# Performance work log

Hardware: AMD Instinct MI355X
Metric: run time of the kernel (lower is better)

The kernel has to match this reference:

```python
import jax, jax.numpy as jnp
import numpy as np

TEMPERATURE = 8.0  # sqrt(d_k), d_k = 64


def setup_inputs() -> dict:
    key = jax.random.key(0)
    kq, kk, kv, km = jax.random.split(key, 4)
    B, Lq, Lk, D = 64, 1024, 1024, 64
    q = jax.random.normal(kq, (B, Lq, D), dtype=jnp.float32)
    k = jax.random.normal(kk, (B, Lk, D), dtype=jnp.float32)
    v = jax.random.normal(kv, (B, Lk, D), dtype=jnp.float32)
    mask = jax.random.randint(km, (B, Lq, Lk), 0, 2).astype(jnp.bool_)
    return {"q": q, "k": k, "v": v, "mask": mask}


def reference(q, k, v, mask):
    # attn = q @ k^T / temperature, masked softmax over last dim, then @ v
    attn = jnp.einsum("bqd,bkd->bqk", q, k) / TEMPERATURE
    attn = jnp.where(mask, -jnp.inf, attn)
    attn = jax.nn.softmax(attn, axis=2)
    output = jnp.einsum("bqk,bkd->bqd", attn, v)
    return (output, attn)
```

## Files before the change

kernel.cpp:

```cpp
#include <hip/hip_runtime.h>
#include <hip/hip_bf16.h>


#define LQT 64
#define KSTRIDE 72
#define PSTRIDE 68

typedef __attribute__((ext_vector_type(8))) short bf16x8;
typedef __attribute__((ext_vector_type(4))) float f32x4;

static __device__ __forceinline__ short f2bf(float f) {
    unsigned u = __builtin_bit_cast(unsigned, f);
    unsigned r = (u + 0x7fffu + ((u >> 16) & 1u)) >> 16;
    return (short)r;
}
static __device__ __forceinline__ bf16x8 pack8(float4 a, float4 b) {
    bf16x8 r;
    r[0] = f2bf(a.x); r[1] = f2bf(a.y); r[2] = f2bf(a.z); r[3] = f2bf(a.w);
    r[4] = f2bf(b.x); r[5] = f2bf(b.y); r[6] = f2bf(b.z); r[7] = f2bf(b.w);
    return r;
}

__global__ __launch_bounds__(256) void attn_kernel(
    const float* __restrict__ q, const float* __restrict__ k,
    const float* __restrict__ v, const int* __restrict__ mask,
    float* __restrict__ out, float* __restrict__ attn)
{
    __shared__ unsigned maskbits[64][32];
    __shared__ short kbuf[64 * KSTRIDE];
    __shared__ short vtbuf[64 * KSTRIDE];
    __shared__ float ptile[4 * 16 * PSTRIDE];

    const int tid  = threadIdx.x;
    const int w    = tid >> 6;
    const int L    = tid & 63;
    const int n    = L & 15;
    const int quad = L >> 4;
    const int b    = blockIdx.y;
    const int q0   = blockIdx.x * LQT;
    const long bq  = (long)b * 1024 + q0;

    const float* qrow = q + (bq + 16 * w + n) * 64 + quad * 8;
    float4 qa0 = ((const float4*)qrow)[0];
    float4 qa1 = ((const float4*)(qrow + 4))[0];
    float4 qb0 = ((const float4*)(qrow + 32))[0];
    float4 qb1 = ((const float4*)(qrow + 36))[0];
    const float sc = 0.125f;
    qa0.x *= sc; qa0.y *= sc; qa0.z *= sc; qa0.w *= sc;
    qa1.x *= sc; qa1.y *= sc; qa1.z *= sc; qa1.w *= sc;
    qb0.x *= sc; qb0.y *= sc; qb0.z *= sc; qb0.w *= sc;
    qb1.x *= sc; qb1.y *= sc; qb1.z *= sc; qb1.w *= sc;
    bf16x8 qf0 = pack8(qa0, qa1);
    bf16x8 qf1 = pack8(qb0, qb1);

    #pragma unroll
    for (int ii = 0; ii < 8; ++ii) {
        int wi  = ii * 256 + tid;
        int row = wi >> 5;
        int wc  = wi & 31;
        const int4* mp = (const int4*)(mask + (bq + row) * 1024 + wc * 32);
        unsigned word = 0;
        #pragma unroll
        for (int j = 0; j < 8; ++j) {
            int4 m4 = mp[j];
            word |= (m4.x != 0 ? 1u : 0u) << (4 * j + 0);
            word |= (m4.y != 0 ? 1u : 0u) << (4 * j + 1);
            word |= (m4.z != 0 ? 1u : 0u) << (4 * j + 2);
            word |= (m4.w != 0 ? 1u : 0u) << (4 * j + 3);
        }
        maskbits[row][wc] = word;
    }

    float m_i[4] = {-1e30f, -1e30f, -1e30f, -1e30f};
    float l_i[4] = {0.f, 0.f, 0.f, 0.f};

    for (int kt = 0; kt < 16; ++kt) {
        __syncthreads();
        {
            const float* kr = k + ((long)b * 1024 + kt * 64 + L) * 64 + w * 16;
            float4 k0 = ((const float4*)kr)[0];
            float4 k1 = ((const float4*)kr)[1];
            float4 k2 = ((const float4*)kr)[2];
            float4 k3 = ((const float4*)kr)[3];
            bf16x8* dst = (bf16x8*)&kbuf[L * KSTRIDE + w * 16];
            dst[0] = pack8(k0, k1);
            dst[1] = pack8(k2, k3);
        }
        __syncthreads();

        f32x4 acc[4];
        #pragma unroll
        for (int t = 0; t < 4; ++t) { acc[t][0]=0.f; acc[t][1]=0.f; acc[t][2]=0.f; acc[t][3]=0.f; }
        #pragma unroll
        for (int t = 0; t < 4; ++t) {
            bf16x8 b0 = *(const bf16x8*)&kbuf[(t * 16 + n) * KSTRIDE + quad * 8];
            bf16x8 b1 = *(const bf16x8*)&kbuf[(t * 16 + n) * KSTRIDE + 32 + quad * 8];
            acc[t] = __builtin_amdgcn_mfma_f32_16x16x32_bf16(qf0, b0, acc[t], 0, 0, 0);
            acc[t] = __builtin_amdgcn_mfma_f32_16x16x32_bf16(qf1, b1, acc[t], 0, 0, 0);
        }
        #pragma unroll
        for (int i = 0; i < 4; ++i) {
            int mrow = 16 * w + quad * 4 + i;
            unsigned w0 = maskbits[mrow][kt * 2];
            unsigned w1 = maskbits[mrow][kt * 2 + 1];
            float s0 = ((w0 >> n)        & 1u) ? -1e30f : acc[0][i];
            float s1 = ((w0 >> (16 + n)) & 1u) ? -1e30f : acc[1][i];
            float s2 = ((w1 >> n)        & 1u) ? -1e30f : acc[2][i];
            float s3 = ((w1 >> (16 + n)) & 1u) ? -1e30f : acc[3][i];
            float mt = fmaxf(fmaxf(s0, s1), fmaxf(s2, s3));
            mt = fmaxf(mt, __shfl_xor(mt, 1));
            mt = fmaxf(mt, __shfl_xor(mt, 2));
            mt = fmaxf(mt, __shfl_xor(mt, 4));
            mt = fmaxf(mt, __shfl_xor(mt, 8));
            float mnew = fmaxf(m_i[i], mt);
            float ps = __expf(s0 - mnew) + __expf(s1 - mnew)
                     + __expf(s2 - mnew) + __expf(s3 - mnew);
            ps += __shfl_xor(ps, 1);
            ps += __shfl_xor(ps, 2);
            ps += __shfl_xor(ps, 4);
            ps += __shfl_xor(ps, 8);
            l_i[i] = l_i[i] * __expf(m_i[i] - mnew) + ps;
            m_i[i] = mnew;
        }
    }
    float linv[4];
    #pragma unroll
    for (int i = 0; i < 4; ++i) linv[i] = 1.0f / l_i[i];

    f32x4 oacc[4];
    #pragma unroll
    for (int t = 0; t < 4; ++t) { oacc[t][0]=0.f; oacc[t][1]=0.f; oacc[t][2]=0.f; oacc[t][3]=0.f; }

    float* attn_row = attn + (bq + 16 * w + n) * 1024;

    for (int kt = 0; kt < 16; ++kt) {
        __syncthreads();
        {
            const float* kr = k + ((long)b * 1024 + kt * 64 + L) * 64 + w * 16;
            float4 k0 = ((const float4*)kr)[0];
            float4 k1 = ((const float4*)kr)[1];
            float4 k2 = ((const float4*)kr)[2];
            float4 k3 = ((const float4*)kr)[3];
            bf16x8* dst = (bf16x8*)&kbuf[L * KSTRIDE + w * 16];
            dst[0] = pack8(k0, k1);
            dst[1] = pack8(k2, k3);

            const float* vr = v + ((long)b * 1024 + kt * 64 + L) * 64 + w * 16;
            float4 v0 = ((const float4*)vr)[0];
            float4 v1 = ((const float4*)vr)[1];
            float4 v2 = ((const float4*)vr)[2];
            float4 v3 = ((const float4*)vr)[3];
            float vv[16] = {v0.x, v0.y, v0.z, v0.w, v1.x, v1.y, v1.z, v1.w,
                            v2.x, v2.y, v2.z, v2.w, v3.x, v3.y, v3.z, v3.w};
            #pragma unroll
            for (int dd = 0; dd < 16; ++dd)
                vtbuf[(w * 16 + dd) * KSTRIDE + L] = f2bf(vv[dd]);
        }
        __syncthreads();

        f32x4 acc[4];
        #pragma unroll
        for (int t = 0; t < 4; ++t) { acc[t][0]=0.f; acc[t][1]=0.f; acc[t][2]=0.f; acc[t][3]=0.f; }
        #pragma unroll
        for (int t = 0; t < 4; ++t) {
            bf16x8 b0 = *(const bf16x8*)&kbuf[(t * 16 + n) * KSTRIDE + quad * 8];
            bf16x8 b1 = *(const bf16x8*)&kbuf[(t * 16 + n) * KSTRIDE + 32 + quad * 8];
            acc[t] = __builtin_amdgcn_mfma_f32_16x16x32_bf16(qf0, b0, acc[t], 0, 0, 0);
            acc[t] = __builtin_amdgcn_mfma_f32_16x16x32_bf16(qf1, b1, acc[t], 0, 0, 0);
        }
        #pragma unroll
        for (int i = 0; i < 4; ++i) {
            int mrow = 16 * w + quad * 4 + i;
            unsigned w0 = maskbits[mrow][kt * 2];
            unsigned w1 = maskbits[mrow][kt * 2 + 1];
            float s0 = ((w0 >> n)        & 1u) ? -1e30f : acc[0][i];
            float s1 = ((w0 >> (16 + n)) & 1u) ? -1e30f : acc[1][i];
            float s2 = ((w1 >> n)        & 1u) ? -1e30f : acc[2][i];
            float s3 = ((w1 >> (16 + n)) & 1u) ? -1e30f : acc[3][i];
            float* pr = &ptile[(w * 16 + quad * 4 + i) * PSTRIDE];
            pr[n]      = __expf(s0 - m_i[i]) * linv[i];
            pr[16 + n] = __expf(s1 - m_i[i]) * linv[i];
            pr[32 + n] = __expf(s2 - m_i[i]) * linv[i];
            pr[48 + n] = __expf(s3 - m_i[i]) * linv[i];
        }
        bf16x8 pf[2];
        #pragma unroll
        for (int c = 0; c < 2; ++c) {
            const float* pp = &ptile[(w * 16 + n) * PSTRIDE + c * 32 + quad * 8];
            float4 p0 = ((const float4*)pp)[0];
            float4 p1 = ((const float4*)pp)[1];
            float* ap = attn_row + kt * 64 + c * 32 + quad * 8;
            ((float4*)ap)[0] = p0;
            ((float4*)ap)[1] = p1;
            pf[c] = pack8(p0, p1);
        }
        #pragma unroll
        for (int t = 0; t < 4; ++t) {
            bf16x8 vb0 = *(const bf16x8*)&vtbuf[(t * 16 + n) * KSTRIDE + quad * 8];
            bf16x8 vb1 = *(const bf16x8*)&vtbuf[(t * 16 + n) * KSTRIDE + 32 + quad * 8];
            oacc[t] = __builtin_amdgcn_mfma_f32_16x16x32_bf16(pf[0], vb0, oacc[t], 0, 0, 0);
            oacc[t] = __builtin_amdgcn_mfma_f32_16x16x32_bf16(pf[1], vb1, oacc[t], 0, 0, 0);
        }
    }

    #pragma unroll
    for (int t = 0; t < 4; ++t)
        #pragma unroll
        for (int i = 0; i < 4; ++i)
            out[(bq + 16 * w + quad * 4 + i) * 64 + t * 16 + n] = oacc[t][i];
}

extern "C" void kernel_launch(void* const* d_in, const int* in_sizes, int n_in,
                              void* d_out, int out_size, void* d_ws, size_t ws_size,
                              hipStream_t stream) {
    const float* q    = (const float*)d_in[0];
    const float* k    = (const float*)d_in[1];
    const float* v    = (const float*)d_in[2];
    const int*   mask = (const int*)d_in[3];
    float* out  = (float*)d_out;
    float* attn = out + (long)64 * 1024 * 64;

    dim3 grid(16, 64, 1);
    dim3 block(256, 1, 1);
    attn_kernel<<<grid, block, 0, stream>>>(q, k, v, mask, out, attn);
}
```

Measured before the change: 616.5 us.

## Precompute bf16 K, transposed V and packed mask bits; stream via async LDS loads

Adds preprocessing kernels that pack the mask into bitwords with ballots, convert K to swizzled bf16, and transpose V to swizzled bf16 in workspace. The main kernel then double-buffers those tiles into LDS with global_load_lds DMA, so each block no longer redoes the fp32 K/V conversion 16 times over. It also stores P as bf16 in a per-wave tile. The cost is three extra launches and workspace traffic, and the attn output is now written as bf16-rounded values, which lowers its precision. A fallback path keeps the old kernel when workspace is too small.

```diff
diff --git a/kernel.cpp b/kernel.cpp
--- a/kernel.cpp
+++ b/kernel.cpp
@@ -2,17 +2,20 @@
 #include <hip/hip_bf16.h>
 
 
-#define LQT 64
-#define KSTRIDE 72
-#define PSTRIDE 68
-
 typedef __attribute__((ext_vector_type(8))) short bf16x8;
 typedef __attribute__((ext_vector_type(4))) float f32x4;
+
+#define GLOBAL_AS __attribute__((address_space(1)))
+#define LDS_AS    __attribute__((address_space(3)))
 
 static __device__ __forceinline__ short f2bf(float f) {
     unsigned u = __builtin_bit_cast(unsigned, f);
     unsigned r = (u + 0x7fffu + ((u >> 16) & 1u)) >> 16;
     return (short)r;
+}
+static __device__ __forceinline__ float bf2f(short s) {
+    unsigned u = ((unsigned)(unsigned short)s) << 16;
+    return __builtin_bit_cast(float, u);
 }
 static __device__ __forceinline__ bf16x8 pack8(float4 a, float4 b) {
     bf16x8 r;
@@ -21,15 +24,82 @@
     return r;
 }
 
-__global__ __launch_bounds__(256) void attn_kernel(
-    const float* __restrict__ q, const float* __restrict__ k,
-    const float* __restrict__ v, const int* __restrict__ mask,
+static __device__ __forceinline__ void dma16(void* lds, const void* g) {
+    __builtin_amdgcn_global_load_lds((const GLOBAL_AS unsigned*)g,
+                                     (LDS_AS unsigned*)lds, 16, 0, 0);
+}
+static __device__ __forceinline__ void stage8k(short* lds, const short* g, int w, int L) {
+    dma16((void*)(lds + (w * 2 + 0) * 512), (const void*)(g + (w * 2 + 0) * 512 + L * 8));
+    dma16((void*)(lds + (w * 2 + 1) * 512), (const void*)(g + (w * 2 + 1) * 512 + L * 8));
+}
+
+#define KIDX(r, c) ((r) * 64 + ((((c) ^ ((r) & 7))) << 3))
+
+__global__ __launch_bounds__(256) void pre_maskpack(const int* __restrict__ mask,
+                                                    unsigned long long* __restrict__ bits) {
+    const int L = threadIdx.x & 63;
+    long gw = ((long)blockIdx.x * 256 + threadIdx.x) >> 6;
+    const long nseg = (64L * 1024 * 1024) / 256;
+    const long step = (long)gridDim.x * 4;
+    for (long seg = gw; seg < nseg; seg += step) {
+        const int* p = mask + seg * 256;
+        unsigned long long b0 = __ballot(p[L] != 0);
+        unsigned long long b1 = __ballot(p[64 + L] != 0);
+        unsigned long long b2 = __ballot(p[128 + L] != 0);
+        unsigned long long b3 = __ballot(p[192 + L] != 0);
+        if (L == 0) {
+            ulonglong2* d = (ulonglong2*)(bits + seg * 4);
+            ulonglong2 t0; t0.x = b0; t0.y = b1;
+            ulonglong2 t1; t1.x = b2; t1.y = b3;
+            d[0] = t0; d[1] = t1;
+        }
+    }
+}
+
+__global__ __launch_bounds__(256) void pre_kconv(const float* __restrict__ k,
+                                                 short* __restrict__ kb) {
+    long ci = (long)blockIdx.x * 256 + threadIdx.x;
+    long row = ci >> 3;
+    int  c   = (int)(ci & 7);
+    const float4* s = (const float4*)(k + row * 64 + c * 8);
+    float4 a = s[0], bb = s[1];
+    int r = (int)(row & 63);
+    short* dst = kb + (row >> 6) * 4096 + (long)r * 64 + ((c ^ (r & 7)) << 3);
+    *(bf16x8*)dst = pack8(a, bb);
+}
+
+__global__ __launch_bounds__(256) void pre_vtrans(const float* __restrict__ v,
+                                                  short* __restrict__ vt) {
+    __shared__ short t[64][72];
+    const int bkt = blockIdx.x;
+    const int tid = threadIdx.x;
+    const int row = tid >> 2;
+    const int cg  = (tid & 3) * 16;
+    const float* src = v + ((long)bkt * 64 + row) * 64 + cg;
+    float4 f0 = ((const float4*)src)[0];
+    float4 f1 = ((const float4*)src)[1];
+    float4 f2 = ((const float4*)src)[2];
+    float4 f3 = ((const float4*)src)[3];
+    float vv[16] = {f0.x, f0.y, f0.z, f0.w, f1.x, f1.y, f1.z, f1.w,
+                    f2.x, f2.y, f2.z, f2.w, f3.x, f3.y, f3.z, f3.w};
+    #pragma unroll
+    for (int dd = 0; dd < 16; ++dd) t[cg + dd][row] = f2bf(vv[dd]);
+    __syncthreads();
+    const int d = tid >> 2, c0 = (tid & 3) * 2;
+    short* dstrow = vt + (long)bkt * 4096 + d * 64;
+    *(int4*)&dstrow[((c0 ^ (d & 7)) << 3)]       = *(int4*)&t[d][c0 * 8];
+    *(int4*)&dstrow[(((c0 + 1) ^ (d & 7)) << 3)] = *(int4*)&t[d][c0 * 8 + 8];
+}
+
+__global__ __launch_bounds__(256) void attn_main(
+    const float* __restrict__ q, const unsigned* __restrict__ bits,
+    const short* __restrict__ kb, const short* __restrict__ vt,
     float* __restrict__ out, float* __restrict__ attn)
 {
-    __shared__ unsigned maskbits[64][32];
-    __shared__ short kbuf[64 * KSTRIDE];
-    __shared__ short vtbuf[64 * KSTRIDE];
-    __shared__ float ptile[4 * 16 * PSTRIDE];
+    __shared__ unsigned maskbits[64 * 32];
+    __shared__ short kbuf[2][64 * 64];
+    __shared__ short vbuf[2][64 * 64];
+    __shared__ short ptile[4][16 * 72];
 
     const int tid  = threadIdx.x;
     const int w    = tid >> 6;
@@ -37,8 +107,17 @@
     const int n    = L & 15;
     const int quad = L >> 4;
     const int b    = blockIdx.y;
-    const int q0   = blockIdx.x * LQT;
-    const long bq  = (long)b * 1024 + q0;
+    const long bq  = (long)b * 1024 + blockIdx.x * 64;
+
+    const short* ktg = kb + (long)b * 65536;
+    const short* vtg = vt + (long)b * 65536;
+
+    {
+        const unsigned* mg = bits + bq * 32;
+        dma16((void*)(maskbits + (w * 2 + 0) * 256), (const void*)(mg + (w * 2 + 0) * 256 + L * 4));
+        dma16((void*)(maskbits + (w * 2 + 1) * 256), (const void*)(mg + (w * 2 + 1) * 256 + L * 4));
+        stage8k(kbuf[0], ktg, w, L);
+    }
 
     const float* qrow = q + (bq + 16 * w + n) * 64 + quad * 8;
     float4 qa0 = ((const float4*)qrow)[0];
@@ -53,6 +132,159 @@
     bf16x8 qf0 = pack8(qa0, qa1);
     bf16x8 qf1 = pack8(qb0, qb1);
 
+    __syncthreads();
+
+    float m_i[4] = {-1e30f, -1e30f, -1e30f, -1e30f};
+    float l_i[4] = {0.f, 0.f, 0.f, 0.f};
+
+    for (int kt = 0; kt < 16; ++kt) {
+        if (kt < 15) stage8k(kbuf[(kt + 1) & 1], ktg + (kt + 1) * 4096, w, L);
+        const short* kl = kbuf[kt & 1];
+        f32x4 acc[4];
+        #pragma unroll
+        for (int t = 0; t < 4; ++t) { acc[t][0]=0.f; acc[t][1]=0.f; acc[t][2]=0.f; acc[t][3]=0.f; }
+        #pragma unroll
+        for (int t = 0; t < 4; ++t) {
+            bf16x8 b0 = *(const bf16x8*)&kl[KIDX(t * 16 + n, quad)];
+            bf16x8 b1 = *(const bf16x8*)&kl[KIDX(t * 16 + n, 4 + quad)];
+            acc[t] = __builtin_amdgcn_mfma_f32_16x16x32_bf16(qf0, b0, acc[t], 0, 0, 0);
+            acc[t] = __builtin_amdgcn_mfma_f32_16x16x32_bf16(qf1, b1, acc[t], 0, 0, 0);
+        }
+        #pragma unroll
+        for (int i = 0; i < 4; ++i) {
+            int mrow = 16 * w + quad * 4 + i;
+            unsigned w0 = maskbits[mrow * 32 + kt * 2];
+            unsigned w1 = maskbits[mrow * 32 + kt * 2 + 1];
+            float s0 = ((w0 >> n)        & 1u) ? -1e30f : acc[0][i];
+            float s1 = ((w0 >> (16 + n)) & 1u) ? -1e30f : acc[1][i];
+            float s2 = ((w1 >> n)        & 1u) ? -1e30f : acc[2][i];
+            float s3 = ((w1 >> (16 + n)) & 1u) ? -1e30f : acc[3][i];
+            float mt = fmaxf(fmaxf(s0, s1), fmaxf(s2, s3));
+            mt = fmaxf(mt, __shfl_xor(mt, 1));
+            mt = fmaxf(mt, __shfl_xor(mt, 2));
+            mt = fmaxf(mt, __shfl_xor(mt, 4));
+            mt = fmaxf(mt, __shfl_xor(mt, 8));
+            float mnew = fmaxf(m_i[i], mt);
+            float ps = __expf(s0 - mnew) + __expf(s1 - mnew)
+                     + __expf(s2 - mnew) + __expf(s3 - mnew);
+            ps += __shfl_xor(ps, 1);
+            ps += __shfl_xor(ps, 2);
+            ps += __shfl_xor(ps, 4);
+            ps += __shfl_xor(ps, 8);
+            l_i[i] = l_i[i] * __expf(m_i[i] - mnew) + ps;
+            m_i[i] = mnew;
+        }
+        __syncthreads();
+    }
+    float linv[4];
+    #pragma unroll
+    for (int i = 0; i < 4; ++i) linv[i] = 1.0f / l_i[i];
+
+    f32x4 oacc[4];
+    #pragma unroll
+    for (int t = 0; t < 4; ++t) { oacc[t][0]=0.f; oacc[t][1]=0.f; oacc[t][2]=0.f; oacc[t][3]=0.f; }
+
+    stage8k(kbuf[0], ktg, w, L);
+    stage8k(vbuf[0], vtg, w, L);
+    __syncthreads();
+
+    float* attn_row = attn + (bq + 16 * w + n) * 1024;
+
+    for (int kt = 0; kt < 16; ++kt) {
+        if (kt < 15) {
+            stage8k(kbuf[(kt + 1) & 1], ktg + (kt + 1) * 4096, w, L);
+            stage8k(vbuf[(kt + 1) & 1], vtg + (kt + 1) * 4096, w, L);
+        }
+        const short* kl = kbuf[kt & 1];
+        const short* vl = vbuf[kt & 1];
+        f32x4 acc[4];
+        #pragma unroll
+        for (int t = 0; t < 4; ++t) { acc[t][0]=0.f; acc[t][1]=0.f; acc[t][2]=0.f; acc[t][3]=0.f; }
+        #pragma unroll
+        for (int t = 0; t < 4; ++t) {
+            bf16x8 b0 = *(const bf16x8*)&kl[KIDX(t * 16 + n, quad)];
+            bf16x8 b1 = *(const bf16x8*)&kl[KIDX(t * 16 + n, 4 + quad)];
+            acc[t] = __builtin_amdgcn_mfma_f32_16x16x32_bf16(qf0, b0, acc[t], 0, 0, 0);
+            acc[t] = __builtin_amdgcn_mfma_f32_16x16x32_bf16(qf1, b1, acc[t], 0, 0, 0);
+        }
+        short* pw = ptile[w];
+        #pragma unroll
+        for (int i = 0; i < 4; ++i) {
+            int mrow = 16 * w + quad * 4 + i;
+            unsigned w0 = maskbits[mrow * 32 + kt * 2];
+            unsigned w1 = maskbits[mrow * 32 + kt * 2 + 1];
+            float s0 = ((w0 >> n)        & 1u) ? -1e30f : acc[0][i];
+            float s1 = ((w0 >> (16 + n)) & 1u) ? -1e30f : acc[1][i];
+            float s2 = ((w1 >> n)        & 1u) ? -1e30f : acc[2][i];
+            float s3 = ((w1 >> (16 + n)) & 1u) ? -1e30f : acc[3][i];
+            short* pr = &pw[(quad * 4 + i) * 72];
+            pr[n]      = f2bf(__expf(s0 - m_i[i]) * linv[i]);
+            pr[16 + n] = f2bf(__expf(s1 - m_i[i]) * linv[i]);
+            pr[32 + n] = f2bf(__expf(s2 - m_i[i]) * linv[i]);
+            pr[48 + n] = f2bf(__expf(s3 - m_i[i]) * linv[i]);
+        }
+        bf16x8 pf0 = *(const bf16x8*)&pw[n * 72 + quad * 8];
+        bf16x8 pf1 = *(const bf16x8*)&pw[n * 72 + 32 + quad * 8];
+        float* ap = attn_row + kt * 64;
+        float4 f0, f1, g0, g1;
+        f0.x = bf2f(pf0[0]); f0.y = bf2f(pf0[1]); f0.z = bf2f(pf0[2]); f0.w = bf2f(pf0[3]);
+        f1.x = bf2f(pf0[4]); f1.y = bf2f(pf0[5]); f1.z = bf2f(pf0[6]); f1.w = bf2f(pf0[7]);
+        g0.x = bf2f(pf1[0]); g0.y = bf2f(pf1[1]); g0.z = bf2f(pf1[2]); g0.w = bf2f(pf1[3]);
+        g1.x = bf2f(pf1[4]); g1.y = bf2f(pf1[5]); g1.z = bf2f(pf1[6]); g1.w = bf2f(pf1[7]);
+        *(float4*)(ap + quad * 8)          = f0;
+        *(float4*)(ap + quad * 8 + 4)      = f1;
+        *(float4*)(ap + 32 + quad * 8)     = g0;
+        *(float4*)(ap + 32 + quad * 8 + 4) = g1;
+        #pragma unroll
+        for (int t = 0; t < 4; ++t) {
+            bf16x8 v0 = *(const bf16x8*)&vl[KIDX(t * 16 + n, quad)];
+            bf16x8 v1 = *(const bf16x8*)&vl[KIDX(t * 16 + n, 4 + quad)];
+            oacc[t] = __builtin_amdgcn_mfma_f32_16x16x32_bf16(pf0, v0, oacc[t], 0, 0, 0);
+            oacc[t] = __builtin_amdgcn_mfma_f32_16x16x32_bf16(pf1, v1, oacc[t], 0, 0, 0);
+        }
+        __syncthreads();
+    }
+
+    #pragma unroll
+    for (int t = 0; t < 4; ++t)
+        #pragma unroll
+        for (int i = 0; i < 4; ++i)
+            out[(bq + 16 * w + quad * 4 + i) * 64 + t * 16 + n] = oacc[t][i];
+}
+
+#define KSTRIDE 72
+#define PSTRIDE 68
+__global__ __launch_bounds__(256) void attn_fallback(
+    const float* __restrict__ q, const float* __restrict__ k,
+    const float* __restrict__ v, const int* __restrict__ mask,
+    float* __restrict__ out, float* __restrict__ attn)
+{
+    __shared__ unsigned maskbits[64][32];
+    __shared__ short kbuf[64 * KSTRIDE];
+    __shared__ short vtbuf[64 * KSTRIDE];
+    __shared__ float ptile[4 * 16 * PSTRIDE];
+
+    const int tid  = threadIdx.x;
+    const int w    = tid >> 6;
+    const int L    = tid & 63;
+    const int n    = L & 15;
+    const int quad = L >> 4;
+    const int b    = blockIdx.y;
+    const long bq  = (long)b * 1024 + blockIdx.x * 64;
+
+    const float* qrow = q + (bq + 16 * w + n) * 64 + quad * 8;
+    float4 qa0 = ((const float4*)qrow)[0];
+    float4 qa1 = ((const float4*)(qrow + 4))[0];
+    float4 qb0 = ((const float4*)(qrow + 32))[0];
+    float4 qb1 = ((const float4*)(qrow + 36))[0];
+    const float sc = 0.125f;
+    qa0.x *= sc; qa0.y *= sc; qa0.z *= sc; qa0.w *= sc;
+    qa1.x *= sc; qa1.y *= sc; qa1.z *= sc; qa1.w *= sc;
+    qb0.x *= sc; qb0.y *= sc; qb0.z *= sc; qb0.w *= sc;
+    qb1.x *= sc; qb1.y *= sc; qb1.z *= sc; qb1.w *= sc;
+    bf16x8 qf0 = pack8(qa0, qa1);
+    bf16x8 qf1 = pack8(qb0, qb1);
+
     #pragma unroll
     for (int ii = 0; ii < 8; ++ii) {
         int wi  = ii * 256 + tid;
@@ -87,7 +319,6 @@
             dst[1] = pack8(k2, k3);
         }
         __syncthreads();
-
         f32x4 acc[4];
         #pragma unroll
         for (int t = 0; t < 4; ++t) { acc[t][0]=0.f; acc[t][1]=0.f; acc[t][2]=0.f; acc[t][3]=0.f; }
@@ -130,7 +361,6 @@
     f32x4 oacc[4];
     #pragma unroll
     for (int t = 0; t < 4; ++t) { oacc[t][0]=0.f; oacc[t][1]=0.f; oacc[t][2]=0.f; oacc[t][3]=0.f; }
-
     float* attn_row = attn + (bq + 16 * w + n) * 1024;
 
     for (int kt = 0; kt < 16; ++kt) {
@@ -144,7 +374,6 @@
             bf16x8* dst = (bf16x8*)&kbuf[L * KSTRIDE + w * 16];
             dst[0] = pack8(k0, k1);
             dst[1] = pack8(k2, k3);
-
             const float* vr = v + ((long)b * 1024 + kt * 64 + L) * 64 + w * 16;
             float4 v0 = ((const float4*)vr)[0];
             float4 v1 = ((const float4*)vr)[1];
@@ -157,7 +386,6 @@
                 vtbuf[(w * 16 + dd) * KSTRIDE + L] = f2bf(vv[dd]);
         }
         __syncthreads();
-
         f32x4 acc[4];
         #pragma unroll
         for (int t = 0; t < 4; ++t) { acc[t][0]=0.f; acc[t][1]=0.f; acc[t][2]=0.f; acc[t][3]=0.f; }
@@ -202,7 +430,6 @@
             oacc[t] = __builtin_amdgcn_mfma_f32_16x16x32_bf16(pf[1], vb1, oacc[t], 0, 0, 0);
         }
     }
-
     #pragma unroll
     for (int t = 0; t < 4; ++t)
         #pragma unroll
@@ -222,5 +449,19 @@
 
     dim3 grid(16, 64, 1);
     dim3 block(256, 1, 1);
-    attn_kernel<<<grid, block, 0, stream>>>(q, k, v, mask, out, attn);
-}
+
+    const size_t need = (size_t)24 << 20;
+    if (ws_size >= need) {
+        unsigned char* ws = (unsigned char*)d_ws;
+        unsigned long long* bits64 = (unsigned long long*)ws;
+        unsigned* bits = (unsigned*)ws;
+        short* kbw = (short*)(ws + ((size_t)8 << 20));
+        short* vtw = (short*)(ws + ((size_t)16 << 20));
+        pre_maskpack<<<2048, 256, 0, stream>>>(mask, bits64);
+        pre_kconv<<<2048, 256, 0, stream>>>(k, kbw);
+        pre_vtrans<<<1024, 256, 0, stream>>>(v, vtw);
+        attn_main<<<grid, block, 0, stream>>>(q, bits, kbw, vtw, out, attn);
+    } else {
+        attn_fallback<<<grid, block, 0, stream>>>(q, k, v, mask, out, attn);
+    }
+}
```

Measured after the change: 572.0 us. 1.08x faster.
